# Kernel optimization log

Hardware: AMD Instinct MI355X
Metric: run time of the kernel (lower is better)

## Reference

```python
import jax, jax.numpy as jnp
import numpy as np

B, S, D, H = 2, 2048, 1024, 16
DH = D // H
DFF = 4 * D
EPS = 1e-5


def layer_norm(x, w, b):
    m = jnp.mean(x, axis=-1, keepdims=True)
    v = jnp.mean((x - m) ** 2, axis=-1, keepdims=True)
    return (x - m) / jnp.sqrt(v + EPS) * w + b


def setup_inputs() -> dict:
    key = jax.random.key(0)
    ks = jax.random.split(key, 12)
    s = 0.02
    x = jax.random.normal(ks[0], (B, S, D), dtype=jnp.float32)
    mask = jnp.tril(jnp.ones((S, S), dtype=jnp.int32))  # causal mask, 0 = blocked
    Wq = jax.random.normal(ks[1], (H, D, DH), dtype=jnp.float32) * s
    Wk = jax.random.normal(ks[2], (H, D, DH), dtype=jnp.float32) * s
    Wv = jax.random.normal(ks[3], (H, D, DH), dtype=jnp.float32) * s
    Wo = jax.random.normal(ks[4], (D, D), dtype=jnp.float32) * s
    bo = jnp.zeros((D,), dtype=jnp.float32)
    W1 = jax.random.normal(ks[5], (D, DFF), dtype=jnp.float32) * s
    b1 = jnp.zeros((DFF,), dtype=jnp.float32)
    W2 = jax.random.normal(ks[6], (DFF, D), dtype=jnp.float32) * s
    b2 = jnp.zeros((D,), dtype=jnp.float32)
    ln1_w = jnp.ones((D,), dtype=jnp.float32)
    ln1_b = jnp.zeros((D,), dtype=jnp.float32)
    ln2_w = jnp.ones((D,), dtype=jnp.float32)
    ln2_b = jnp.zeros((D,), dtype=jnp.float32)
    return {"x": x, "mask": mask, "Wq": Wq, "Wk": Wk, "Wv": Wv, "Wo": Wo,
            "bo": bo, "W1": W1, "b1": b1, "W2": W2, "b2": b2,
            "ln1_w": ln1_w, "ln1_b": ln1_b, "ln2_w": ln2_w, "ln2_b": ln2_b}


def reference(x, mask, Wq, Wk, Wv, Wo, bo, W1, b1, W2, b2,
              ln1_w, ln1_b, ln2_w, ln2_b):
    # --- pre-LN attention ---
    xn = layer_norm(x, ln1_w, ln1_b)
    q = jnp.einsum('bsd,hdk->bhsk', xn, Wq)  # [B,H,S,DH]
    k = jnp.einsum('bsd,hdk->bhsk', xn, Wk)
    v = jnp.einsum('bsd,hdk->bhsk', xn, Wv)
    scores = jnp.einsum('bhik,bhjk->bhij', q, k) / jnp.sqrt(jnp.float32(DH))
    scores = jnp.where(mask == 0, jnp.float32(-1e9), scores)  # mask broadcasts [S,S]->[B,H,S,S]
    attn = jax.nn.softmax(scores, axis=-1)
    o = jnp.einsum('bhij,bhjk->bhik', attn, v)        # [B,H,S,DH]
    o = o.transpose(0, 2, 1, 3).reshape(x.shape[0], x.shape[1], D)  # concat heads
    attn_out = o @ Wo + bo
    x = x + attn_out
    # --- pre-LN FFN ---
    xn2 = layer_norm(x, ln2_w, ln2_b)
    h = jax.nn.relu(xn2 @ W1 + b1)
    x = x + (h @ W2 + b2)
    return x
```

## Files before the change

kernel.cpp:

```cpp
#include <hip/hip_runtime.h>
#include <hip/hip_bf16.h>
#include <stdint.h>

#define DEV static __device__ __forceinline__

using f32x4  = __attribute__((ext_vector_type(4))) float;
using bf16x4 = __attribute__((ext_vector_type(4))) __bf16;
using bf16x8 = __attribute__((ext_vector_type(8))) __bf16;

constexpr int SEQ = 2048;

DEV unsigned short f2bf(float f) {
  union { float f; unsigned u; } c; c.f = f;
  unsigned u = c.u;
  u += 0x7fffu + ((u >> 16) & 1u);
  return (unsigned short)(u >> 16);
}

DEV float wred_sum(float v) {
  #pragma unroll
  for (int m = 32; m > 0; m >>= 1) v += __shfl_xor(v, m, 64);
  return v;
}

DEV void g2l16(const unsigned short* g, unsigned short* l) {
  __builtin_amdgcn_global_load_lds(
      (const __attribute__((address_space(1))) void*)g,
      (__attribute__((address_space(3))) void*)l, 16, 0, 0);
}

DEV int xcd_map(int bid, int nwg) {
  const int cpx = nwg >> 3;
  return (bid & 7) * cpx + (bid >> 3);
}

__global__ __launch_bounds__(256) void convw_all(
    const float* __restrict__ Wq, const float* __restrict__ Wk,
    const float* __restrict__ Wv, const float* __restrict__ Wo,
    const float* __restrict__ W1, const float* __restrict__ W2,
    unsigned short* __restrict__ WqkvT, unsigned short* __restrict__ WoT,
    unsigned short* __restrict__ W1T,   unsigned short* __restrict__ W2T)
{
  const int blk = blockIdx.x;
  const float* in; unsigned short* out; int K, Nh, n0, k0, hsel = 0;
  if (blk < 3072) {
    const int seg = blk >> 10, l = blk & 1023;
    in  = seg == 0 ? Wq : seg == 1 ? Wk : Wv;
    out = WqkvT + (size_t)seg * 1024 * 1024;
    K = 1024; Nh = 64;
    n0 = (l & 1) * 32; k0 = ((l >> 1) & 31) * 32; hsel = l >> 6;
  } else if (blk < 4096) {
    const int l = blk - 3072; in = Wo; out = WoT; K = 1024; Nh = 1024;
    n0 = (l & 31) * 32; k0 = (l >> 5) * 32;
  } else if (blk < 8192) {
    const int l = blk - 4096; in = W1; out = W1T; K = 1024; Nh = 4096;
    n0 = (l & 127) * 32; k0 = (l >> 7) * 32;
  } else {
    const int l = blk - 8192; in = W2; out = W2T; K = 4096; Nh = 1024;
    n0 = (l & 31) * 32; k0 = (l >> 5) * 32;
  }
  const float* inh = in + (size_t)hsel * K * Nh;
  unsigned short* outh = out + (size_t)hsel * Nh * K;
  __shared__ float t[32][33];
  const int tx = threadIdx.x & 31, ty = threadIdx.x >> 5;
  #pragma unroll
  for (int r = 0; r < 32; r += 8)
    t[ty + r][tx] = inh[(size_t)(k0 + ty + r) * Nh + (n0 + tx)];
  __syncthreads();
  #pragma unroll
  for (int r = 0; r < 32; r += 8)
    outh[(size_t)(n0 + ty + r) * K + (k0 + tx)] = f2bf(t[tx][ty + r]);
}

__global__ __launch_bounds__(256) void ln_kernel(
    const float* __restrict__ x, const float* __restrict__ w,
    const float* __restrict__ b, unsigned short* __restrict__ out)
{
  const int row = blockIdx.x;
  const int tid = threadIdx.x;
  const float4 v = ((const float4*)(x + (size_t)row * 1024))[tid];
  float s  = v.x + v.y + v.z + v.w;
  float s2 = v.x*v.x + v.y*v.y + v.z*v.z + v.w*v.w;
  s = wred_sum(s); s2 = wred_sum(s2);
  __shared__ float rs[4], rs2[4];
  const int wave = tid >> 6, lane = tid & 63;
  if (lane == 0) { rs[wave] = s; rs2[wave] = s2; }
  __syncthreads();
  const float S  = rs[0] + rs[1] + rs[2] + rs[3];
  const float S2 = rs2[0] + rs2[1] + rs2[2] + rs2[3];
  const float mean = S * (1.f / 1024.f);
  const float var  = S2 * (1.f / 1024.f) - mean * mean;
  const float inv  = rsqrtf(var + 1e-5f);
  const float4 wv = ((const float4*)w)[tid];
  const float4 bv = ((const float4*)b)[tid];
  ushort4 o;
  o.x = f2bf((v.x - mean) * inv * wv.x + bv.x);
  o.y = f2bf((v.y - mean) * inv * wv.y + bv.y);
  o.z = f2bf((v.z - mean) * inv * wv.z + bv.z);
  o.w = f2bf((v.w - mean) * inv * wv.w + bv.w);
  ((ushort4*)(out + (size_t)row * 1024))[tid] = o;
}

template<int EPI>
__global__ __launch_bounds__(256) void gemm_kp(
    const unsigned short* __restrict__ A, const unsigned short* __restrict__ BT,
    void* __restrict__ Cout, const float* __restrict__ bias,
    const float* __restrict__ res, int M, int N, int K)
{
  __shared__ unsigned short sA[3][128 * 64];
  __shared__ unsigned short sB[3][64 * 64];
  const int tid = threadIdx.x;
  const int wave = tid >> 6, lane = tid & 63;
  const int wr = wave >> 1, wc = wave & 1;
  const int bid = xcd_map(blockIdx.y * gridDim.x + blockIdx.x, gridDim.x * gridDim.y);
  const int m0 = (bid / gridDim.x) * 128, n0 = (bid % gridDim.x) * 64;
  const int lr = lane & 15, lg = lane >> 4;
  const int wb = tid & 192;

  const f32x4 zero = {0.f, 0.f, 0.f, 0.f};
  f32x4 acc[4][2];
  #pragma unroll
  for (int i = 0; i < 4; ++i)
    #pragma unroll
    for (int j = 0; j < 2; ++j) acc[i][j] = zero;

  auto STAGE = [&](int slot, int kt) {
    const int k0 = kt * 64;
    #pragma unroll
    for (int r = 0; r < 4; ++r) {
      const int c = tid + 256 * r;
      const int row = c >> 3;
      const int so = ((c & 7) ^ (row & 7)) * 8;
      g2l16(A + (size_t)(m0 + row) * K + k0 + so, sA[slot] + (size_t)(wb + 256 * r) * 8);
    }
    #pragma unroll
    for (int r = 0; r < 2; ++r) {
      const int c = tid + 256 * r;
      const int row = c >> 3;
      const int so = ((c & 7) ^ (row & 7)) * 8;
      g2l16(BT + (size_t)(n0 + row) * K + k0 + so, sB[slot] + (size_t)(wb + 256 * r) * 8);
    }
  };

  const int nt = K / 64;
  STAGE(0, 0); STAGE(1, 1);

  for (int t = 0; t < nt; ++t) {
    asm volatile("s_waitcnt vmcnt(6)" ::: "memory");
    __builtin_amdgcn_s_barrier();
    const int slot = t % 3;
    bf16x8 af[4][2], bfr[2][2];
    #pragma unroll
    for (int i = 0; i < 4; ++i) {
      const int row = wr * 64 + i * 16 + lr;
      #pragma unroll
      for (int kk = 0; kk < 2; ++kk)
        af[i][kk] = *(const bf16x8*)(sA[slot] + row * 64 + (((kk * 4 + lg) ^ (row & 7)) << 3));
    }
    #pragma unroll
    for (int j = 0; j < 2; ++j) {
      const int row = wc * 32 + j * 16 + lr;
      #pragma unroll
      for (int kk = 0; kk < 2; ++kk)
        bfr[j][kk] = *(const bf16x8*)(sB[slot] + row * 64 + (((kk * 4 + lg) ^ (row & 7)) << 3));
    }
    __builtin_amdgcn_s_setprio(1);
    #pragma unroll
    for (int i = 0; i < 4; ++i)
      #pragma unroll
      for (int j = 0; j < 2; ++j)
        #pragma unroll
        for (int kk = 0; kk < 2; ++kk)
          acc[i][j] = __builtin_amdgcn_mfma_f32_16x16x32_bf16(af[i][kk], bfr[j][kk], acc[i][j], 0, 0, 0);
    __builtin_amdgcn_s_setprio(0);
    const int nx = (t + 2 < nt) ? t + 2 : nt - 1;
    STAGE((t + 2) % 3, nx);
  }
  asm volatile("s_waitcnt vmcnt(0)" ::: "memory");

  #pragma unroll
  for (int i = 0; i < 4; ++i) {
    #pragma unroll
    for (int j = 0; j < 2; ++j) {
      #pragma unroll
      for (int r = 0; r < 4; ++r) {
        const int row = m0 + wr * 64 + i * 16 + lg * 4 + r;
        const int col = n0 + wc * 32 + j * 16 + lr;
        const float v = acc[i][j][r];
        if (EPI == 1) {
          ((float*)Cout)[(size_t)row * N + col] = v + bias[col] + res[(size_t)row * N + col];
        } else {
          ((unsigned short*)Cout)[(size_t)row * N + col] = f2bf(v);
        }
      }
    }
  }
}

template<int EPI>
__global__ __launch_bounds__(512) void gemm256(
    const unsigned short* __restrict__ A, const unsigned short* __restrict__ BT,
    void* __restrict__ Cout, const float* __restrict__ bias,
    int M, int N, int K)
{
  __shared__ unsigned short sA[2][256 * 64];
  __shared__ unsigned short sB[2][256 * 64];
  const int tid = threadIdx.x;
  const int lane = tid & 63;
  const int wave = tid >> 6;
  const int wm = wave >> 2, wn = wave & 3;
  const int bid = xcd_map(blockIdx.y * gridDim.x + blockIdx.x, gridDim.x * gridDim.y);
  const int m0 = (bid / gridDim.x) * 256, n0 = (bid % gridDim.x) * 256;
  const int lr = lane & 15, lg = lane >> 4;

  const f32x4 zero = {0.f, 0.f, 0.f, 0.f};
  f32x4 acc[8][4];
  #pragma unroll
  for (int i = 0; i < 8; ++i)
    #pragma unroll
    for (int j = 0; j < 4; ++j) acc[i][j] = zero;

  auto STAGE = [&](int buf, int k0) {
    #pragma unroll
    for (int r = 0; r < 4; ++r) {
      const int c = tid + 512 * r;
      const int row = c >> 3;
      const int slot = (c & 7) ^ (row & 7);
      const int cb = (tid & 448) + 512 * r;
      g2l16(A  + (size_t)(m0 + row) * K + k0 + slot * 8, sA[buf] + (size_t)cb * 8);
      g2l16(BT + (size_t)(n0 + row) * K + k0 + slot * 8, sB[buf] + (size_t)cb * 8);
    }
  };
  auto RD = [&](const unsigned short* base, int R, int C) -> const bf16x8* {
    return (const bf16x8*)(base + R * 64 + ((((C >> 3) ^ (R & 7))) << 3));
  };

  const int nt = K / 64;
  STAGE(0, 0);
  asm volatile("s_waitcnt vmcnt(0)" ::: "memory");
  __syncthreads();

  for (int t = 0; t < nt; ++t) {
    const int buf = t & 1;
    if (t + 1 < nt) STAGE(buf ^ 1, (t + 1) * 64);
    #pragma unroll
    for (int p = 0; p < 4; ++p) {
      const int ih = p >> 1, jh = p & 1;
      bf16x8 af[4][2], bfr[2][2];
      #pragma unroll
      for (int i = 0; i < 4; ++i)
        #pragma unroll
        for (int kk = 0; kk < 2; ++kk)
          af[i][kk] = *RD(sA[buf], wm * 128 + (ih * 4 + i) * 16 + lr, kk * 32 + lg * 8);
      #pragma unroll
      for (int j = 0; j < 2; ++j)
        #pragma unroll
        for (int kk = 0; kk < 2; ++kk)
          bfr[j][kk] = *RD(sB[buf], wn * 64 + (jh * 2 + j) * 16 + lr, kk * 32 + lg * 8);
      __builtin_amdgcn_s_setprio(1);
      #pragma unroll
      for (int i = 0; i < 4; ++i)
        #pragma unroll
        for (int j = 0; j < 2; ++j)
          #pragma unroll
          for (int kk = 0; kk < 2; ++kk)
            acc[ih * 4 + i][jh * 2 + j] = __builtin_amdgcn_mfma_f32_16x16x32_bf16(
                af[i][kk], bfr[j][kk], acc[ih * 4 + i][jh * 2 + j], 0, 0, 0);
      __builtin_amdgcn_s_setprio(0);
      if (p < 3) __builtin_amdgcn_s_barrier();
    }
    asm volatile("s_waitcnt vmcnt(0)" ::: "memory");
    __builtin_amdgcn_s_barrier();
  }

  #pragma unroll
  for (int i = 0; i < 8; ++i) {
    #pragma unroll
    for (int j = 0; j < 4; ++j) {
      #pragma unroll
      for (int r = 0; r < 4; ++r) {
        const int row = m0 + wm * 128 + i * 16 + lg * 4 + r;
        const int col = n0 + wn * 64 + j * 16 + lr;
        float v = acc[i][j][r];
        if (EPI == 0) {
          if (col < 1024) v *= 0.18033688f;
          ((unsigned short*)Cout)[(size_t)row * N + col] = f2bf(v);
        } else {
          float t2 = v + bias[col];
          t2 = t2 > 0.f ? t2 : 0.f;
          ((unsigned short*)Cout)[(size_t)row * N + col] = f2bf(t2);
        }
      }
    }
  }
}

constexpr int VPAD = 136;

__global__ __launch_bounds__(512) void attn_mfma(
    const unsigned short* __restrict__ qkv, unsigned short* __restrict__ o)
{
  const int p  = blockIdx.x >> 5;
  const int bh = blockIdx.x & 31;
  const int b = bh >> 4, h = bh & 15;
  const int tid = threadIdx.x;
  const int wave = tid >> 6, lane = tid & 63;
  const int grp = wave >> 2, wv = wave & 3;
  const int lr = lane & 15, lg = lane >> 4;

  const int qi = grp ? p : (31 - p);
  const int mynt = (qi >> 1) + 1;
  const int nt_long = ((31 - p) >> 1) + 1;
  const int q0 = qi * 64;

  __shared__ unsigned short Ks[128 * 64];
  __shared__ unsigned short Vs[64 * VPAD];
  __shared__ unsigned short Ps[8][16 * VPAD];

  const size_t qbase = ((size_t)(b * SEQ + q0 + wv * 16 + lr)) * 3072 + h * 64;
  bf16x8 qb[2];
  qb[0] = *(const bf16x8*)(qkv + qbase + lg * 8);
  qb[1] = *(const bf16x8*)(qkv + qbase + 32 + lg * 8);

  const f32x4 zero = {0.f, 0.f, 0.f, 0.f};
  f32x4 o_acc[4];
  #pragma unroll
  for (int dn = 0; dn < 4; ++dn) o_acc[dn] = zero;
  float m_run = -1e30f, l_run = 0.f;

  for (int t = 0; t < nt_long; ++t) {
    const int j0 = t * 128;
    __syncthreads();
    #pragma unroll
    for (int r = 0; r < 2; ++r) {
      const int c = tid + 512 * r;
      const int row = c >> 3;
      const int slot = (c & 7) ^ (row & 7);
      const size_t gsrc = ((size_t)(b * SEQ + j0 + row)) * 3072 + 1024 + h * 64 + slot * 8;
      g2l16(qkv + gsrc, Ks + (size_t)((tid & 448) + 512 * r) * 8);
    }
    #pragma unroll
    for (int r = 0; r < 2; ++r) {
      const int c = tid + 512 * r;
      const int key = c & 127, dseg = c >> 7;
      const size_t base = ((size_t)(b * SEQ + j0 + key)) * 3072 + 2048 + h * 64 + dseg * 8;
      int4 rv = *(const int4*)(qkv + base);
      const unsigned short* u = (const unsigned short*)&rv;
      #pragma unroll
      for (int e = 0; e < 8; ++e) Vs[(dseg * 8 + e) * VPAD + key] = u[e];
    }
    __syncthreads();

    if (t < mynt) {
      f32x4 s[8];
      __builtin_amdgcn_s_setprio(1);
      #pragma unroll
      for (int n = 0; n < 8; ++n) {
        const int row = n * 16 + lr;
        const bf16x8 kf0 = *(const bf16x8*)(Ks + row * 64 + ((lg ^ (row & 7)) << 3));
        const bf16x8 kf1 = *(const bf16x8*)(Ks + row * 64 + (((4 + lg) ^ (row & 7)) << 3));
        s[n] = __builtin_amdgcn_mfma_f32_16x16x32_bf16(kf0, qb[0], zero, 0, 0, 0);
        s[n] = __builtin_amdgcn_mfma_f32_16x16x32_bf16(kf1, qb[1], s[n], 0, 0, 0);
      }
      __builtin_amdgcn_s_setprio(0);

      const bool diag = (t == mynt - 1);
      float zm = -3e38f;
      if (diag) {
        const int q = q0 + wv * 16 + lr;
        const int kbase = j0 + lg * 4;
        #pragma unroll
        for (int n = 0; n < 8; ++n)
          #pragma unroll
          for (int r = 0; r < 4; ++r) {
            float z = s[n][r];
            if (kbase + n * 16 + r > q) z = -3e38f;
            s[n][r] = z;
            zm = fmaxf(zm, z);
          }
      } else {
        #pragma unroll
        for (int n = 0; n < 8; ++n)
          zm = fmaxf(fmaxf(fmaxf(zm, s[n][0]), fmaxf(s[n][1], s[n][2])), s[n][3]);
      }
      zm = fmaxf(zm, __shfl_xor(zm, 16, 64));
      zm = fmaxf(zm, __shfl_xor(zm, 32, 64));

      const bool skip = __all(zm - m_run <= 10.f);
      if (!skip) {
        const float mnew = fmaxf(m_run, zm);
        const float alpha = exp2f(m_run - mnew);
        m_run = mnew;
        l_run *= alpha;
        float a4[4];
        #pragma unroll
        for (int r = 0; r < 4; ++r) a4[r] = __shfl(alpha, lg * 4 + r, 64);
        #pragma unroll
        for (int dn = 0; dn < 4; ++dn)
          #pragma unroll
          for (int r = 0; r < 4; ++r) o_acc[dn][r] *= a4[r];
      }

      float psum = 0.f;
      #pragma unroll
      for (int n = 0; n < 8; ++n) {
        float p0 = exp2f(s[n][0] - m_run); psum += p0;
        float p1 = exp2f(s[n][1] - m_run); psum += p1;
        float p2 = exp2f(s[n][2] - m_run); psum += p2;
        float p3 = exp2f(s[n][3] - m_run); psum += p3;
        bf16x4 pw = { (__bf16)p0, (__bf16)p1, (__bf16)p2, (__bf16)p3 };
        *(bf16x4*)(&Ps[wave][lr * VPAD + n * 16 + lg * 4]) = pw;
      }
      psum += __shfl_xor(psum, 16, 64);
      psum += __shfl_xor(psum, 32, 64);
      l_run += psum;

      bf16x8 pa[4];
      #pragma unroll
      for (int kk = 0; kk < 4; ++kk)
        pa[kk] = *(const bf16x8*)(&Ps[wave][lr * VPAD + kk * 32 + lg * 8]);
      __builtin_amdgcn_s_setprio(1);
      #pragma unroll
      for (int dn = 0; dn < 4; ++dn) {
        #pragma unroll
        for (int kk = 0; kk < 4; ++kk) {
          const bf16x8 vf = *(const bf16x8*)(Vs + (dn * 16 + lr) * VPAD + kk * 32 + lg * 8);
          o_acc[dn] = __builtin_amdgcn_mfma_f32_16x16x32_bf16(pa[kk], vf, o_acc[dn], 0, 0, 0);
        }
      }
      __builtin_amdgcn_s_setprio(0);
    }
  }

  float linv[4];
  #pragma unroll
  for (int r = 0; r < 4; ++r) linv[r] = 1.f / __shfl(l_run, lg * 4 + r, 64);
  #pragma unroll
  for (int r = 0; r < 4; ++r) {
    const int qq = q0 + wv * 16 + lg * 4 + r;
    const size_t obase = ((size_t)(b * SEQ + qq)) * 1024 + h * 64;
    #pragma unroll
    for (int dn = 0; dn < 4; ++dn)
      o[obase + dn * 16 + lr] = f2bf(o_acc[dn][r] * linv[r]);
  }
}

extern "C" void kernel_launch(void* const* d_in, const int* in_sizes, int n_in,
                              void* d_out, int out_size, void* d_ws, size_t ws_size,
                              hipStream_t stream) {
  const float* x    = (const float*)d_in[0];
  const float* Wq   = (const float*)d_in[2];
  const float* Wk   = (const float*)d_in[3];
  const float* Wv   = (const float*)d_in[4];
  const float* Wo   = (const float*)d_in[5];
  const float* bo   = (const float*)d_in[6];
  const float* W1   = (const float*)d_in[7];
  const float* b1   = (const float*)d_in[8];
  const float* W2   = (const float*)d_in[9];
  const float* b2   = (const float*)d_in[10];
  const float* ln1w = (const float*)d_in[11];
  const float* ln1b = (const float*)d_in[12];
  const float* ln2w = (const float*)d_in[13];
  const float* ln2b = (const float*)d_in[14];

  char* ws = (char*)d_ws;
  unsigned short* WqkvT = (unsigned short*)(ws);
  unsigned short* WoT   = (unsigned short*)(ws + 6291456);
  unsigned short* W1T   = (unsigned short*)(ws + 8388608);
  unsigned short* W2T   = (unsigned short*)(ws + 16777216);
  unsigned short* xn    = (unsigned short*)(ws + 25165824);
  float*          x1    = (float*)        (ws + 33554432);
  unsigned short* qkv   = (unsigned short*)(ws + 50331648);
  unsigned short* oc    = (unsigned short*)(ws + 75497472);
  unsigned short* hbuf  = qkv;

  convw_all<<<12288, 256, 0, stream>>>(Wq, Wk, Wv, Wo, W1, W2, WqkvT, WoT, W1T, W2T);
  ln_kernel<<<4096, 256, 0, stream>>>(x, ln1w, ln1b, xn);
  gemm256<0><<<dim3(12, 16), 512, 0, stream>>>(xn, WqkvT, qkv, nullptr, 4096, 3072, 1024);
  attn_mfma<<<512, 512, 0, stream>>>(qkv, oc);
  gemm_kp<1><<<dim3(16, 32), 256, 0, stream>>>(oc, WoT, x1, bo, x, 4096, 1024, 1024);
  ln_kernel<<<4096, 256, 0, stream>>>(x1, ln2w, ln2b, xn);
  gemm256<2><<<dim3(16, 16), 512, 0, stream>>>(xn, W1T, hbuf, b1, 4096, 4096, 1024);
  gemm_kp<1><<<dim3(16, 32), 256, 0, stream>>>(hbuf, W2T, (float*)d_out, b2, x1, 4096, 1024, 4096);
}
```

Before: 224.2 us.

## Replace 256x256 GEMM with 128x256 triple-buffered K=32 pipelined kernel

The QKV and FFN1 GEMMs move from a 256x256 tile with double-buffered K=64 stages to a 128x256 tile with a three-slot ring of K=32 stages. Loads now run two stages ahead, with a partial vmcnt wait and one barrier per iteration instead of several. The smaller tile doubles the grid size and frees registers and LDS, allowing more blocks per CU (launch bounds 512,4). The cost is less data reuse per tile and more global traffic for the B operand.

```diff
diff --git a/kernel.cpp b/kernel.cpp
--- a/kernel.cpp
+++ b/kernel.cpp
@@ -198,88 +198,81 @@
 }
 
 template<int EPI>
-__global__ __launch_bounds__(512) void gemm256(
+__global__ __launch_bounds__(512, 4) void gemm_kp2(
     const unsigned short* __restrict__ A, const unsigned short* __restrict__ BT,
     void* __restrict__ Cout, const float* __restrict__ bias,
     int M, int N, int K)
 {
-  __shared__ unsigned short sA[2][256 * 64];
-  __shared__ unsigned short sB[2][256 * 64];
+  __shared__ unsigned short sA[3][128 * 32];
+  __shared__ unsigned short sB[3][256 * 32];
   const int tid = threadIdx.x;
-  const int lane = tid & 63;
-  const int wave = tid >> 6;
+  const int wave = tid >> 6, lane = tid & 63;
   const int wm = wave >> 2, wn = wave & 3;
   const int bid = xcd_map(blockIdx.y * gridDim.x + blockIdx.x, gridDim.x * gridDim.y);
-  const int m0 = (bid / gridDim.x) * 256, n0 = (bid % gridDim.x) * 256;
+  const int m0 = (bid / gridDim.x) * 128, n0 = (bid % gridDim.x) * 256;
   const int lr = lane & 15, lg = lane >> 4;
+  const int wb = tid & 448;
 
   const f32x4 zero = {0.f, 0.f, 0.f, 0.f};
-  f32x4 acc[8][4];
-  #pragma unroll
-  for (int i = 0; i < 8; ++i)
+  f32x4 acc[4][4];
+  #pragma unroll
+  for (int i = 0; i < 4; ++i)
     #pragma unroll
     for (int j = 0; j < 4; ++j) acc[i][j] = zero;
 
-  auto STAGE = [&](int buf, int k0) {
-    #pragma unroll
-    for (int r = 0; r < 4; ++r) {
+  auto STAGE = [&](int slot, int kt) {
+    const int k0 = kt * 32;
+    {
+      const int row = tid >> 2;
+      const int so = ((tid & 3) ^ (row & 3)) * 8;
+      g2l16(A + (size_t)(m0 + row) * K + k0 + so, sA[slot] + (size_t)wb * 8);
+    }
+    #pragma unroll
+    for (int r = 0; r < 2; ++r) {
       const int c = tid + 512 * r;
-      const int row = c >> 3;
-      const int slot = (c & 7) ^ (row & 7);
-      const int cb = (tid & 448) + 512 * r;
-      g2l16(A  + (size_t)(m0 + row) * K + k0 + slot * 8, sA[buf] + (size_t)cb * 8);
-      g2l16(BT + (size_t)(n0 + row) * K + k0 + slot * 8, sB[buf] + (size_t)cb * 8);
+      const int row = c >> 2;
+      const int so = ((c & 3) ^ (row & 3)) * 8;
+      g2l16(BT + (size_t)(n0 + row) * K + k0 + so, sB[slot] + (size_t)(wb + 512 * r) * 8);
     }
   };
-  auto RD = [&](const unsigned short* base, int R, int C) -> const bf16x8* {
-    return (const bf16x8*)(base + R * 64 + ((((C >> 3) ^ (R & 7))) << 3));
-  };
-
-  const int nt = K / 64;
-  STAGE(0, 0);
+
+  const int nt = K / 32;
+  STAGE(0, 0); STAGE(1, 1);
+
+  for (int t = 0; t < nt; ++t) {
+    asm volatile("s_waitcnt vmcnt(3)" ::: "memory");
+    __builtin_amdgcn_s_barrier();
+    const int slot = t % 3;
+    bf16x8 af[4], bfr[4];
+    #pragma unroll
+    for (int i = 0; i < 4; ++i) {
+      const int row = wm * 64 + i * 16 + lr;
+      af[i] = *(const bf16x8*)(sA[slot] + row * 32 + ((lg ^ (row & 3)) << 3));
+    }
+    #pragma unroll
+    for (int j = 0; j < 4; ++j) {
+      const int row = wn * 64 + j * 16 + lr;
+      bfr[j] = *(const bf16x8*)(sB[slot] + row * 32 + ((lg ^ (row & 3)) << 3));
+    }
+    __builtin_amdgcn_s_setprio(1);
+    #pragma unroll
+    for (int i = 0; i < 4; ++i)
+      #pragma unroll
+      for (int j = 0; j < 4; ++j)
+        acc[i][j] = __builtin_amdgcn_mfma_f32_16x16x32_bf16(af[i], bfr[j], acc[i][j], 0, 0, 0);
+    __builtin_amdgcn_s_setprio(0);
+    const int nx = (t + 2 < nt) ? t + 2 : nt - 1;
+    STAGE((t + 2) % 3, nx);
+  }
   asm volatile("s_waitcnt vmcnt(0)" ::: "memory");
-  __syncthreads();
-
-  for (int t = 0; t < nt; ++t) {
-    const int buf = t & 1;
-    if (t + 1 < nt) STAGE(buf ^ 1, (t + 1) * 64);
-    #pragma unroll
-    for (int p = 0; p < 4; ++p) {
-      const int ih = p >> 1, jh = p & 1;
-      bf16x8 af[4][2], bfr[2][2];
-      #pragma unroll
-      for (int i = 0; i < 4; ++i)
-        #pragma unroll
-        for (int kk = 0; kk < 2; ++kk)
-          af[i][kk] = *RD(sA[buf], wm * 128 + (ih * 4 + i) * 16 + lr, kk * 32 + lg * 8);
-      #pragma unroll
-      for (int j = 0; j < 2; ++j)
-        #pragma unroll
-        for (int kk = 0; kk < 2; ++kk)
-          bfr[j][kk] = *RD(sB[buf], wn * 64 + (jh * 2 + j) * 16 + lr, kk * 32 + lg * 8);
-      __builtin_amdgcn_s_setprio(1);
-      #pragma unroll
-      for (int i = 0; i < 4; ++i)
-        #pragma unroll
-        for (int j = 0; j < 2; ++j)
-          #pragma unroll
-          for (int kk = 0; kk < 2; ++kk)
-            acc[ih * 4 + i][jh * 2 + j] = __builtin_amdgcn_mfma_f32_16x16x32_bf16(
-                af[i][kk], bfr[j][kk], acc[ih * 4 + i][jh * 2 + j], 0, 0, 0);
-      __builtin_amdgcn_s_setprio(0);
-      if (p < 3) __builtin_amdgcn_s_barrier();
-    }
-    asm volatile("s_waitcnt vmcnt(0)" ::: "memory");
-    __builtin_amdgcn_s_barrier();
-  }
-
-  #pragma unroll
-  for (int i = 0; i < 8; ++i) {
+
+  #pragma unroll
+  for (int i = 0; i < 4; ++i) {
     #pragma unroll
     for (int j = 0; j < 4; ++j) {
       #pragma unroll
       for (int r = 0; r < 4; ++r) {
-        const int row = m0 + wm * 128 + i * 16 + lg * 4 + r;
+        const int row = m0 + wm * 64 + i * 16 + lg * 4 + r;
         const int col = n0 + wn * 64 + j * 16 + lr;
         float v = acc[i][j][r];
         if (EPI == 0) {
@@ -476,10 +469,10 @@
 
   convw_all<<<12288, 256, 0, stream>>>(Wq, Wk, Wv, Wo, W1, W2, WqkvT, WoT, W1T, W2T);
   ln_kernel<<<4096, 256, 0, stream>>>(x, ln1w, ln1b, xn);
-  gemm256<0><<<dim3(12, 16), 512, 0, stream>>>(xn, WqkvT, qkv, nullptr, 4096, 3072, 1024);
+  gemm_kp2<0><<<dim3(12, 32), 512, 0, stream>>>(xn, WqkvT, qkv, nullptr, 4096, 3072, 1024);
   attn_mfma<<<512, 512, 0, stream>>>(qkv, oc);
   gemm_kp<1><<<dim3(16, 32), 256, 0, stream>>>(oc, WoT, x1, bo, x, 4096, 1024, 1024);
   ln_kernel<<<4096, 256, 0, stream>>>(x1, ln2w, ln2b, xn);
-  gemm256<2><<<dim3(16, 16), 512, 0, stream>>>(xn, W1T, hbuf, b1, 4096, 4096, 1024);
+  gemm_kp2<2><<<dim3(16, 32), 512, 0, stream>>>(xn, W1T, hbuf, b1, 4096, 4096, 1024);
   gemm_kp<1><<<dim3(16, 32), 256, 0, stream>>>(hbuf, W2T, (float*)d_out, b2, x1, 4096, 1024, 4096);
 }
```

Measured after the change: 228.0 us. About the same (+1.7%).
